# Optimization experiments

Hardware: AMD Instinct MI355X
Metric: run time of the kernel (lower is better)

## Reference

```python
import jax, jax.numpy as jnp
import numpy as np

N, E, F_IN, F_E, H = 50000, 800000, 128, 16, 64
NEG_SLOPE = 0.2


def _glorot(key, shape):
    fan_in, fan_out = shape[0], shape[-1]
    lim = np.sqrt(6.0 / (fan_in + fan_out))
    return jax.random.uniform(key, shape, jnp.float32, -lim, lim)


def setup_inputs() -> dict:
    key = jax.random.key(0)
    ks = jax.random.split(key, 24)
    inp = {
        "x": jax.random.normal(ks[0], (N, F_IN), jnp.float32),
        "edge_index": jax.random.randint(ks[1], (2, E), 0, N, jnp.int64),
        "edge_attr": jax.random.normal(ks[2], (E, F_E), jnp.float32),
    }
    k = 3
    for i, f_in in zip((1, 2, 3), (F_IN, H, H)):
        inp[f"W{i}"] = _glorot(ks[k], (f_in, H)); k += 1
        inp[f"as{i}"] = _glorot(ks[k], (H,)); k += 1
        inp[f"ad{i}"] = _glorot(ks[k], (H,)); k += 1
        inp[f"We{i}"] = _glorot(ks[k], (F_E, H)); k += 1
        inp[f"ae{i}"] = _glorot(ks[k], (H,)); k += 1
        inp[f"b{i}"] = jnp.zeros((H,), jnp.float32)
        k += 1
    return inp


def gat_conv(x, src, dst, ea, W, a_s, a_d, We, a_e, b):
    # x: [N, f_in]; src/dst: [E'] (self-loops already appended); ea: [E', F_E]
    n = x.shape[0]
    h = x @ W                                   # [N, H]
    alpha_src = h @ a_s                          # [N]
    alpha_dst = h @ a_d                          # [N]
    alpha_e = (ea @ We) @ a_e                    # [E']
    alpha = alpha_src[src] + alpha_dst[dst] + alpha_e
    alpha = jnp.where(alpha > 0, alpha, NEG_SLOPE * alpha)  # leaky_relu
    # segment softmax over incoming edges of each dst node
    amax = jax.ops.segment_max(alpha, dst, num_segments=n)
    ex = jnp.exp(alpha - amax[dst])
    denom = jax.ops.segment_sum(ex, dst, num_segments=n)
    coef = ex / (denom[dst] + 1e-16)             # [E']
    out = jax.ops.segment_sum(h[src] * coef[:, None], dst, num_segments=n)
    return out + b


def reference(x, edge_index, edge_attr,
              W1, as1, ad1, We1, ae1, b1,
              W2, as2, ad2, We2, ae2, b2,
              W3, as3, ad3, We3, ae3, b3):
    n = x.shape[0]
    # add self-loops (PyG GATConv default), edge_attr fill_value='mean'
    loop = jnp.arange(n, dtype=edge_index.dtype)
    src = jnp.concatenate([edge_index[0], loop])
    dst = jnp.concatenate([edge_index[1], loop])
    ea_mean = jnp.mean(edge_attr, axis=0)
    ea = jnp.concatenate([edge_attr, jnp.broadcast_to(ea_mean, (n, edge_attr.shape[1]))], axis=0)

    x1 = jax.nn.elu(gat_conv(x, src, dst, ea, W1, as1, ad1, We1, ae1, b1))
    x2 = jax.nn.elu(gat_conv(x1, src, dst, ea, W2, as2, ad2, We2, ae2, b2))
    x3 = jax.nn.elu(gat_conv(x2, src, dst, ea, W3, as3, ad3, We3, ae3, b3))
    node_embeddings = x1 + x2 + x3
    graph_embedding = jnp.mean(node_embeddings, axis=0, keepdims=True)  # batch=None path
    return node_embeddings, graph_embedding
```

## Files before the change

kernel.cpp:

```cpp
#include <hip/hip_runtime.h>
#include <hip/hip_fp16.h>
#include <math.h>

#define HD 64
#define MAXNBK 512
#define NPREB 512

typedef unsigned long long u64;
typedef _Float16 f16;
typedef _Float16 f16x8 __attribute__((ext_vector_type(8)));
typedef float f32x4 __attribute__((ext_vector_type(4)));

__device__ __forceinline__ u64 pack_rec(int src, float a0, float a1, float a2) {
    return (u64)(src & 0xFFFF)
         | ((u64)__half_as_ushort(__float2half(a0)) << 16)
         | ((u64)__half_as_ushort(__float2half(a1)) << 32)
         | ((u64)__half_as_ushort(__float2half(a2)) << 48);
}

__global__ void k_init(int* bcnt, float* gacc, int* tick, float* suG,
                       const float* We1, const float* ae1,
                       const float* We2, const float* ae2,
                       const float* We3, const float* ae3, int FE) {
    int t = threadIdx.x;
    for (int i = t; i < MAXNBK; i += 256) bcnt[i] = 0;
    if (t < HD) gacc[t] = 0.f;
    if (t == 0) *tick = 0;
    if (t < 3 * FE) {
        int l = t / FE, f = t % FE;
        const float* We = (l == 0) ? We1 : (l == 1) ? We2 : We3;
        const float* ae = (l == 0) ? ae1 : (l == 1) ? ae2 : ae3;
        float s = 0.f;
        for (int hh = 0; hh < HD; ++hh) s += We[f * HD + hh] * ae[hh];
        suG[t] = s;
    }
}

__global__ void k_pre(const int* __restrict__ ei, const float* __restrict__ ea,
                      const float* __restrict__ suG,
                      int E, int FE, u64* __restrict__ recE,
                      float* __restrict__ partials,
                      int nt, int chunk, int* bcnt, int* __restrict__ bhist, int NBK) {
    extern __shared__ float lds[];
    int t = threadIdx.x;

    if (blockIdx.x >= nt) {
        int* lc = (int*)lds;
        for (int i = t; i < NBK; i += 256) lc[i] = 0;
        __syncthreads();
        int cb = blockIdx.x - nt;
        int lo = cb * chunk, hi = min(E, lo + chunk);
        for (int e = lo + t; e < hi; e += 256)
            atomicAdd(&lc[ei[E + e] >> 7], 1);
        __syncthreads();
        for (int i = t; i < NBK; i += 256) {
            int c = lc[i];
            bhist[(size_t)i * NPREB + cb] = c;
            if (c) atomicAdd(&bcnt[i], c);
        }
        return;
    }

    size_t ebase = (size_t)blockIdx.x * 1024;
    float4 c0 = make_float4(0.f, 0.f, 0.f, 0.f), c1 = c0, c2 = c0, c3 = c0;

#pragma unroll
    for (int k = 0; k < 4; ++k) {
        size_t e = ebase + (size_t)k * 256 + t;
        bool ok = e < (size_t)E;
        size_t ec = ok ? e : (size_t)(E - 1);
        const float4* row = (const float4*)(ea + ec * FE);
        float4 r0 = row[0], r1 = row[1], r2 = row[2], r3 = row[3];
        int src = ei[ec];
        float rr[16];
        *(float4*)&rr[0] = r0; *(float4*)&rr[4] = r1;
        *(float4*)&rr[8] = r2; *(float4*)&rr[12] = r3;
        float a0 = 0.f, a1 = 0.f, a2 = 0.f;
#pragma unroll
        for (int f = 0; f < 16; ++f) {
            float v = rr[f];
            a0 += v * suG[f];
            a1 += v * suG[16 + f];
            a2 += v * suG[32 + f];
        }
        if (ok) {
            c0.x += r0.x; c0.y += r0.y; c0.z += r0.z; c0.w += r0.w;
            c1.x += r1.x; c1.y += r1.y; c1.z += r1.z; c1.w += r1.w;
            c2.x += r2.x; c2.y += r2.y; c2.z += r2.z; c2.w += r2.w;
            c3.x += r3.x; c3.y += r3.y; c3.z += r3.z; c3.w += r3.w;
            recE[e] = pack_rec(src, a0, a1, a2);
        }
    }

    float* cs = lds;
    float* cw = lds + 256 * 17;
    cs[t * 17 + 0] = c0.x; cs[t * 17 + 1] = c0.y; cs[t * 17 + 2] = c0.z; cs[t * 17 + 3] = c0.w;
    cs[t * 17 + 4] = c1.x; cs[t * 17 + 5] = c1.y; cs[t * 17 + 6] = c1.z; cs[t * 17 + 7] = c1.w;
    cs[t * 17 + 8] = c2.x; cs[t * 17 + 9] = c2.y; cs[t * 17 + 10] = c2.z; cs[t * 17 + 11] = c2.w;
    cs[t * 17 + 12] = c3.x; cs[t * 17 + 13] = c3.y; cs[t * 17 + 14] = c3.z; cs[t * 17 + 15] = c3.w;
    __syncthreads();
    if (t < 64) {
        int f = t & 15, g = t >> 4;
        float s = 0.f;
        for (int r = 0; r < 64; ++r) s += cs[(g * 64 + r) * 17 + f];
        cw[t] = s;
    }
    __syncthreads();
    if (t < 16)
        partials[blockIdx.x * 16 + t] = cw[t] + cw[16 + t] + cw[32 + t] + cw[48 + t];
}

__global__ void k_u2(const float* __restrict__ partials, int NB,
                     const float* __restrict__ suG,
                     float* sE, int FE, float invE,
                     const int* __restrict__ bcnt,
                     int* bfill , int* bbase, int NBK, int E) {
    __shared__ float red[256 * 4];
    __shared__ float mea[16];
    __shared__ int ib[256];
    int t = threadIdx.x;
    const float4* p4 = (const float4*)partials;
    int tot4 = NB * 4;
    float4 acc = make_float4(0.f, 0.f, 0.f, 0.f);
    for (int i = t; i < tot4; i += 256) {
        float4 v = p4[i];
        acc.x += v.x; acc.y += v.y; acc.z += v.z; acc.w += v.w;
    }
    red[t * 4 + 0] = acc.x; red[t * 4 + 1] = acc.y;
    red[t * 4 + 2] = acc.z; red[t * 4 + 3] = acc.w;
    int i0 = 2 * t, i1 = 2 * t + 1;
    int c0 = (i0 < NBK) ? bcnt[i0] : 0;
    int c1 = (i1 < NBK) ? bcnt[i1] : 0;
    ib[t] = c0 + c1;
    __syncthreads();
    for (int d = 1; d < 256; d <<= 1) {
        int x = (t >= d) ? ib[t - d] : 0;
        __syncthreads();
        ib[t] += x;
        __syncthreads();
    }
    int excl = ib[t] - (c0 + c1);
    if (i0 < NBK) { bbase[i0] = excl;      bfill[i0 * 16] = excl; }
    if (i1 < NBK) { bbase[i1] = excl + c0; bfill[i1 * 16] = excl + c0; }
    if (t == 0) bbase[NBK] = E;
    if (t < 16) {
        int q = t >> 2, j = t & 3;
        float s = 0.f;
        for (int k = 0; k < 64; ++k) s += red[(q + k * 4) * 4 + j];
        mea[q * 4 + j] = s * invE;
    }
    __syncthreads();
    if (t < 3) {
        float a = 0.f;
        for (int f = 0; f < FE; ++f) a += mea[f] * suG[t * FE + f];
        sE[t] = a;
    }
}

__global__ void k_bucket(const int* __restrict__ ei, const u64* __restrict__ recE,
                         int E, int chunk, int* bfill ,
                         u64* __restrict__ binned, unsigned char* __restrict__ bdstl,
                         int NBK, const int* __restrict__ bhist) {
    __shared__ int gb[MAXNBK], lrank[MAXNBK];
    int t = threadIdx.x;
    int cb = blockIdx.x;
    for (int i = t; i < NBK; i += 256) {
        int c = bhist[(size_t)i * NPREB + cb];
        lrank[i] = 0;
        gb[i] = c ? atomicAdd(&bfill[i * 16], c) : 0;
    }
    __syncthreads();
    int lo = cb * chunk, hi = min(E, lo + chunk);
    for (int e = lo + t; e < hi; e += 256) {
        u64 r = recE[e];
        int dst = ei[E + e];
        int b = dst >> 7;
        int rank = atomicAdd(&lrank[b], 1);
        int pos = gb[b] + rank;
        binned[pos] = r;
        bdstl[pos] = (unsigned char)(dst & 127);
    }
}

__global__ void k_sort(const int* __restrict__ bbase, const u64* __restrict__ binned,
                       const unsigned char* __restrict__ bdstl,
                       const float* __restrict__ sE,
                       int* __restrict__ row_ptr,
                       u64* __restrict__ rec, int N, int E) {
    __shared__ int lcnt[128], lfill[128];
    int b = blockIdx.x, t = threadIdx.x;
    int base = bbase[b], nrec = bbase[b + 1] - base;
    if (t < 128) lcnt[t] = 0;
    __syncthreads();
    for (int i = t; i < nrec; i += 256)
        atomicAdd(&lcnt[bdstl[base + i]], 1);
    __syncthreads();
    int v = (t < 128) ? lcnt[t] : 0;
    for (int d = 1; d < 128; d <<= 1) {
        int x = (t >= d && t < 128) ? lcnt[t - d] : 0;
        __syncthreads();
        if (t < 128) lcnt[t] += x;
        __syncthreads();
    }
    int gnode = (b << 7) + t;
    if (t < 128) {
        int rp = base + gnode + (lcnt[t] - v);
        if (gnode < N) {
            row_ptr[gnode] = rp;
            rec[rp] = pack_rec(gnode, sE[0], sE[1], sE[2]);
        }
        lfill[t] = rp + 1;
    }
    if (b == 0 && t == 0) row_ptr[N] = E + N;
    __syncthreads();
    for (int i = t; i < nrec; i += 256) {
        u64 r = binned[base + i];
        int dl = bdstl[base + i];
        int p = atomicAdd(&lfill[dl], 1);
        rec[p] = r;
    }
}

__global__ void k_gemm(const void* __restrict__ xin, int in_f16,
                       const float* __restrict__ W,
                       const float* __restrict__ a_s, const float* __restrict__ a_d,
                       __half* __restrict__ h, float* __restrict__ as_n,
                       float* __restrict__ ad_n, int N, int K) {
    extern __shared__ char smem[];
    const int SK = K + 8;
    f16* xs = (f16*)smem;
    f16* wt = xs + 64 * SK;
    int t = threadIdx.x;
    int nb = blockIdx.x * 64;

    int nK4 = K >> 2;
    if (in_f16) {
        const __half* xh = (const __half*)xin;
        for (int i = t; i < 64 * nK4; i += 256) {
            int row = i / nK4, c4 = i % nK4;
            int gr = nb + row; if (gr >= N) gr = N - 1;
            u64 v = ((const u64*)(xh + (size_t)gr * K))[c4];
            *(u64*)&xs[row * SK + c4 * 4] = v;
        }
    } else {
        const float* xf = (const float*)xin;
        for (int i = t; i < 64 * nK4; i += 256) {
            int row = i / nK4, c4 = i % nK4;
            int gr = nb + row; if (gr >= N) gr = N - 1;
            float4 v = ((const float4*)(xf + (size_t)gr * K))[c4];
            f16* p = &xs[row * SK + c4 * 4];
            p[0] = (f16)v.x; p[1] = (f16)v.y; p[2] = (f16)v.z; p[3] = (f16)v.w;
        }
    }
    for (int i = t; i < K * 64; i += 256) {
        int k = i >> 6, c = i & 63;
        wt[c * SK + k] = (f16)W[i];
    }
    __syncthreads();

    int wv = t >> 6, lane = t & 63;
    int m = lane & 15, quad = lane >> 4;
    int rowA = wv * 16 + m;

    f32x4 acc[4];
#pragma unroll
    for (int ct = 0; ct < 4; ++ct) acc[ct] = (f32x4){0.f, 0.f, 0.f, 0.f};

    for (int ks = 0; ks < (K >> 5); ++ks) {
        f16x8 a = *(const f16x8*)&xs[rowA * SK + ks * 32 + quad * 8];
#pragma unroll
        for (int ct = 0; ct < 4; ++ct) {
            f16x8 bf = *(const f16x8*)&wt[(ct * 16 + m) * SK + ks * 32 + quad * 8];
            acc[ct] = __builtin_amdgcn_mfma_f32_16x16x32_f16(a, bf, acc[ct], 0, 0, 0);
        }
    }

    {
        float as_c[4], ad_c[4];
#pragma unroll
        for (int ct = 0; ct < 4; ++ct) {
            as_c[ct] = a_s[ct * 16 + m];
            ad_c[ct] = a_d[ct * 16 + m];
        }
#pragma unroll
        for (int r = 0; r < 4; ++r) {
            float ps = acc[0][r] * as_c[0] + acc[1][r] * as_c[1]
                     + acc[2][r] * as_c[2] + acc[3][r] * as_c[3];
            float pd = acc[0][r] * ad_c[0] + acc[1][r] * ad_c[1]
                     + acc[2][r] * ad_c[2] + acc[3][r] * ad_c[3];
#pragma unroll
            for (int dd = 8; dd; dd >>= 1) {
                ps += __shfl_xor(ps, dd, 64);
                pd += __shfl_xor(pd, dd, 64);
            }
            if (m == 0) {
                int gr = nb + wv * 16 + quad * 4 + r;
                if (gr < N) { as_n[gr] = ps; ad_n[gr] = pd; }
            }
        }
    }

    __syncthreads();
    f16* ht = xs;
    const int HS = 72;
#pragma unroll
    for (int ct = 0; ct < 4; ++ct)
#pragma unroll
        for (int r = 0; r < 4; ++r) {
            int rl = wv * 16 + quad * 4 + r;
            ht[rl * HS + ct * 16 + m] = (f16)acc[ct][r];
        }
    __syncthreads();

    {
        int row = t >> 2, cb = (t & 3) * 16;
        int gr = nb + row;
        if (gr < N) {
            ulonglong2 v0 = *(const ulonglong2*)&ht[row * HS + cb];
            ulonglong2 v1 = *(const ulonglong2*)&ht[row * HS + cb + 8];
            *(ulonglong2*)(h + (size_t)gr * HD + cb) = v0;
            *(ulonglong2*)(h + (size_t)gr * HD + cb + 8) = v1;
        }
    }
}

__global__ void k_aggr(const __half* __restrict__ h, const float* __restrict__ as_n,
                       const float* __restrict__ ad_n, const int* __restrict__ row_ptr,
                       const u64* __restrict__ rec, int l,
                       const float* __restrict__ b, __half* __restrict__ x_out,
                       float* __restrict__ emb, int N, int first) {
    int wave = threadIdx.x >> 6, lane = threadIdx.x & 63;
    int hl = lane & 31;
    int n = blockIdx.x * 8 + wave * 2 + (lane >> 5);
    int nc = min(n, N - 1);
    int base = row_ptr[nc], end = row_ptr[nc + 1];
    float adv = ad_n[nc];
    const int shift = 16 * (l + 1);
    int qq = (lane >> 3) & 3, fo = lane & 7;
    int nch = (end - base + 31) >> 5;
    int nchmax = max(nch, __shfl_xor(nch, 32, 64));
    float m = -INFINITY, d = 0.f;
    float acc[8];
#pragma unroll
    for (int k = 0; k < 8; ++k) acc[k] = 0.f;

    for (int ch = 0; ch < nchmax; ++ch) {
        int c = base + (ch << 5);
        int cnt = min(32, end - c);
        float a = -INFINITY;
        int s = 0;
        if (hl < cnt) {
            u64 r = rec[c + hl];
            s = (int)(r & 0xFFFFull);
            float aE = __half2float(__ushort_as_half((unsigned short)(r >> shift)));
            a = as_n[s] + adv + aE;
            a = (a > 0.f) ? a : 0.2f * a;
        }
        float mc = a;
#pragma unroll
        for (int dd = 16; dd; dd >>= 1) mc = fmaxf(mc, __shfl_xor(mc, dd, 64));
        float mn = fmaxf(m, mc);
        float w = (hl < cnt) ? __expf(a - mn) : 0.f;
        float dc = w;
#pragma unroll
        for (int dd = 16; dd; dd >>= 1) dc += __shfl_xor(dc, dd, 64);
        float sc = __expf(m - mn);
        d = d * sc + dc;
#pragma unroll
        for (int k = 0; k < 8; ++k) acc[k] *= sc;
        m = mn;
        int iters = (max(cnt, 0) + 3) >> 2;
        for (int j4 = 0; j4 < iters; ++j4) {
            int j = (j4 << 2) + qq;
            int sl = (lane & 32) + j;
            int sj = __shfl(s, sl, 64);
            float wj = __shfl(w, sl, 64);
            uint4 hv = *(const uint4*)(h + (size_t)sj * HD + (fo << 3));
            asm("v_fma_mix_f32 %0, %1, %2, %0 op_sel:[0,0,0] op_sel_hi:[0,1,0]"
                : "+v"(acc[0]) : "v"(wj), "v"(hv.x));
            asm("v_fma_mix_f32 %0, %1, %2, %0 op_sel:[0,1,0] op_sel_hi:[0,1,0]"
                : "+v"(acc[1]) : "v"(wj), "v"(hv.x));
            asm("v_fma_mix_f32 %0, %1, %2, %0 op_sel:[0,0,0] op_sel_hi:[0,1,0]"
                : "+v"(acc[2]) : "v"(wj), "v"(hv.y));
            asm("v_fma_mix_f32 %0, %1, %2, %0 op_sel:[0,1,0] op_sel_hi:[0,1,0]"
                : "+v"(acc[3]) : "v"(wj), "v"(hv.y));
            asm("v_fma_mix_f32 %0, %1, %2, %0 op_sel:[0,0,0] op_sel_hi:[0,1,0]"
                : "+v"(acc[4]) : "v"(wj), "v"(hv.z));
            asm("v_fma_mix_f32 %0, %1, %2, %0 op_sel:[0,1,0] op_sel_hi:[0,1,0]"
                : "+v"(acc[5]) : "v"(wj), "v"(hv.z));
            asm("v_fma_mix_f32 %0, %1, %2, %0 op_sel:[0,0,0] op_sel_hi:[0,1,0]"
                : "+v"(acc[6]) : "v"(wj), "v"(hv.w));
            asm("v_fma_mix_f32 %0, %1, %2, %0 op_sel:[0,1,0] op_sel_hi:[0,1,0]"
                : "+v"(acc[7]) : "v"(wj), "v"(hv.w));
        }
    }

#pragma unroll
    for (int k = 0; k < 8; ++k) {
        acc[k] += __shfl_xor(acc[k], 8, 64);
        acc[k] += __shfl_xor(acc[k], 16, 64);
    }
    if (hl < 8 && n < N) {
        float inv = 1.f / (d + 1e-16f);
        const float4* b4p = (const float4*)(b + (fo << 3));
        float4 b0 = b4p[0], b1 = b4p[1];
        float bb[8] = {b0.x, b0.y, b0.z, b0.w, b1.x, b1.y, b1.z, b1.w};
        float vv[8];
#pragma unroll
        for (int k = 0; k < 8; ++k) {
            float v = acc[k] * inv + bb[k];
            vv[k] = (v > 0.f) ? v : expm1f(v);
        }
        union { unsigned short us[8]; ulonglong2 u2; } ou;
#pragma unroll
        for (int k = 0; k < 8; ++k) ou.us[k] = __half_as_ushort(__float2half(vv[k]));
        *(ulonglong2*)(x_out + (size_t)n * HD + (fo << 3)) = ou.u2;
        float4* ep = (float4*)(emb + (size_t)n * HD + (fo << 3));
        if (first) {
            ep[0] = make_float4(vv[0], vv[1], vv[2], vv[3]);
            ep[1] = make_float4(vv[4], vv[5], vv[6], vv[7]);
        } else {
            float4 e0 = ep[0], e1 = ep[1];
            e0.x += vv[0]; e0.y += vv[1]; e0.z += vv[2]; e0.w += vv[3];
            e1.x += vv[4]; e1.y += vv[5]; e1.z += vv[6]; e1.w += vv[7];
            ep[0] = e0; ep[1] = e1;
        }
    }
}

__global__ void k_red(float* __restrict__ emb, float* __restrict__ gacc,
                      int* __restrict__ tick, int N) {
    __shared__ float lds[256];
    __shared__ int lastf;
    int f = threadIdx.x & 63, w = threadIdx.x >> 6;
    float s = 0.f;
    for (int n = blockIdx.x * 4 + w; n < N; n += gridDim.x * 4)
        s += emb[(size_t)n * HD + f];
    lds[threadIdx.x] = s;
    __syncthreads();
    if (w == 0) {
        float v = lds[f] + lds[64 + f] + lds[128 + f] + lds[192 + f];
        atomicAdd(&gacc[f], v);
    }
    __syncthreads();
    __threadfence();
    if (threadIdx.x == 0)
        lastf = (atomicAdd(tick, 1) == (int)gridDim.x - 1);
    __syncthreads();
    if (lastf && threadIdx.x < HD) {
        float g = __hip_atomic_load(&gacc[threadIdx.x], __ATOMIC_RELAXED,
                                    __HIP_MEMORY_SCOPE_AGENT);
        emb[(size_t)N * HD + threadIdx.x] = g / (float)N;
    }
}

extern "C" void kernel_launch(void* const* d_in, const int* in_sizes, int n_in,
                              void* d_out, int out_size, void* d_ws, size_t ws_size,
                              hipStream_t stream) {
    const float* x = (const float*)d_in[0];
    const int* ei = (const int*)d_in[1];
    const float* ea = (const float*)d_in[2];

    const int FIN = in_sizes[3] / HD;
    const int N = in_sizes[0] / FIN;
    const int E = in_sizes[1] / 2;
    const int FE = in_sizes[2] / E;
    const int NBK = (N + 127) >> 7;

    const float* W[3];  const float* as_[3]; const float* ad_[3];
    const float* We[3]; const float* ae_[3]; const float* bb[3];
    for (int l = 0; l < 3; ++l) {
        W[l]  = (const float*)d_in[3 + 6 * l + 0];
        as_[l] = (const float*)d_in[3 + 6 * l + 1];
        ad_[l] = (const float*)d_in[3 + 6 * l + 2];
        We[l] = (const float*)d_in[3 + 6 * l + 3];
        ae_[l] = (const float*)d_in[3 + 6 * l + 4];
        bb[l] = (const float*)d_in[3 + 6 * l + 5];
    }

    int ntiles = (E + 1023) / 1024;
    int chunk = (E + NPREB - 1) / NPREB;

    char* ws = (char*)d_ws;
    size_t off = 0;
    auto alloc = [&](size_t bytes) {
        void* p = ws + off;
        off += (bytes + 255) & ~(size_t)255;
        return p;
    };
    __half* h      = (__half*)alloc((size_t)N * HD * 2);
    __half* x_cur  = (__half*)alloc((size_t)N * HD * 2);
    float*  as_n   = (float*)alloc((size_t)N * 4);
    float*  ad_n   = (float*)alloc((size_t)N * 4);
    int*    rowp   = (int*)alloc((size_t)(N + 1) * 4);
    int*    bcnt   = (int*)alloc((size_t)MAXNBK * 4);
    int*    bfill  = (int*)alloc((size_t)MAXNBK * 16 * 4);
    int*    bbase  = (int*)alloc((size_t)(MAXNBK + 1) * 4);
    int*    bhist  = (int*)alloc((size_t)MAXNBK * NPREB * 4);
    u64*    rec    = (u64*)alloc((size_t)(E + N) * 8);
    u64*    recE   = (u64*)alloc((size_t)E * 8);
    u64*    binned = (u64*)alloc((size_t)E * 8);
    unsigned char* bdstl = (unsigned char*)alloc((size_t)E);
    float*  partials = (float*)alloc((size_t)ntiles * 16 * 4);
    float*  sE     = (float*)alloc(3 * 4);
    float*  gacc   = (float*)alloc(HD * 4);
    float*  suG    = (float*)alloc(3 * 16 * 4);
    int*    tick   = (int*)alloc(4);
    (void)ws_size; (void)n_in; (void)out_size;

    float* emb = (float*)d_out;

    k_init<<<1, 256, 0, stream>>>(bcnt, gacc, tick, suG,
                                  We[0], ae_[0], We[1], ae_[1], We[2], ae_[2], FE);
    size_t pre_lds = (size_t)(256 * 17 + 64) * 4;
    k_pre<<<ntiles + NPREB, 256, pre_lds, stream>>>(ei, ea, suG, E, FE, recE, partials,
                                                    ntiles, chunk, bcnt, bhist, NBK);
    k_u2<<<1, 256, 0, stream>>>(partials, ntiles, suG, sE, FE, 1.0f / (float)E,
                                bcnt, bfill, bbase, NBK, E);
    k_bucket<<<NPREB, 256, 0, stream>>>(ei, recE, E, chunk, bfill, binned, bdstl,
                                        NBK, bhist);
    k_sort<<<NBK, 256, 0, stream>>>(bbase, binned, bdstl, sE, rowp, rec, N, E);

    for (int l = 0; l < 3; ++l) {
        const void* xin = (l == 0) ? (const void*)x : (const void*)x_cur;
        int in_f16 = (l == 0) ? 0 : 1;
        int K = (l == 0) ? FIN : HD;
        size_t ldsz = (size_t)(2 * 64 * (K + 8)) * 2;
        k_gemm<<<(N + 63) / 64, 256, ldsz, stream>>>(xin, in_f16, W[l], as_[l], ad_[l],
                                                     h, as_n, ad_n, N, K);
        k_aggr<<<(N + 7) / 8, 256, 0, stream>>>(h, as_n, ad_n, rowp, rec, l,
                                                bb[l], x_cur, emb, N, (l == 0) ? 1 : 0);
    }

    k_red<<<256, 256, 0, stream>>>(emb, gacc, tick, N);
}
```

Baseline: 344.5 us.

## Fuse layer-1 GEMM into preprocessing launch and pre-transpose weights once

```diff
diff --git a/kernel.cpp b/kernel.cpp
--- a/kernel.cpp
+++ b/kernel.cpp
@@ -21,7 +21,9 @@
 __global__ void k_init(int* bcnt, float* gacc, int* tick, float* suG,
                        const float* We1, const float* ae1,
                        const float* We2, const float* ae2,
-                       const float* We3, const float* ae3, int FE) {
+                       const float* We3, const float* ae3, int FE,
+                       const float* W1, const float* W2, const float* W3,
+                       f16* WT0, f16* WT1, f16* WT2, int FIN) {
     int t = threadIdx.x;
     for (int i = t; i < MAXNBK; i += 256) bcnt[i] = 0;
     if (t < HD) gacc[t] = 0.f;
@@ -34,21 +36,116 @@
         for (int hh = 0; hh < HD; ++hh) s += We[f * HD + hh] * ae[hh];
         suG[t] = s;
     }
-}
-
-__global__ void k_pre(const int* __restrict__ ei, const float* __restrict__ ea,
-                      const float* __restrict__ suG,
-                      int E, int FE, u64* __restrict__ recE,
-                      float* __restrict__ partials,
-                      int nt, int chunk, int* bcnt, int* __restrict__ bhist, int NBK) {
-    extern __shared__ float lds[];
+    for (int i = t; i < HD * FIN; i += 256) {
+        int k = i >> 6, c = i & 63;
+        WT0[c * FIN + k] = (f16)W1[i];
+    }
+    for (int i = t; i < HD * HD; i += 256) {
+        int k = i >> 6, c = i & 63;
+        WT1[c * HD + k] = (f16)W2[i];
+        WT2[c * HD + k] = (f16)W3[i];
+    }
+}
+
+__global__ void k_preX(const int* __restrict__ ei, const float* __restrict__ ea,
+                       const float* __restrict__ suG,
+                       int E, int FE, u64* __restrict__ recE,
+                       float* __restrict__ partials,
+                       int nt, int chunk, int* bcnt, int* __restrict__ bhist, int NBK,
+                       int Gg, const float* __restrict__ x,
+                       const f16* __restrict__ WT,
+                       const float* __restrict__ a_s, const float* __restrict__ a_d,
+                       __half* __restrict__ h, float* __restrict__ as_n,
+                       float* __restrict__ ad_n, int N, int K) {
+    extern __shared__ char smemraw[];
     int t = threadIdx.x;
 
-    if (blockIdx.x >= nt) {
-        int* lc = (int*)lds;
+    if (blockIdx.x < Gg) {
+        const int SK = K + 8;
+        f16* xs = (f16*)smemraw;
+        int nb = blockIdx.x * 64;
+        int nK4 = K >> 2;
+        for (int i = t; i < 64 * nK4; i += 256) {
+            int row = i / nK4, c4 = i % nK4;
+            int gr = nb + row; if (gr >= N) gr = N - 1;
+            float4 v = ((const float4*)(x + (size_t)gr * K))[c4];
+            f16* p = &xs[row * SK + c4 * 4];
+            p[0] = (f16)v.x; p[1] = (f16)v.y; p[2] = (f16)v.z; p[3] = (f16)v.w;
+        }
+        __syncthreads();
+
+        int wv = t >> 6, lane = t & 63;
+        int m = lane & 15, quad = lane >> 4;
+        int rowA = wv * 16 + m;
+
+        f32x4 acc[4];
+#pragma unroll
+        for (int ct = 0; ct < 4; ++ct) acc[ct] = (f32x4){0.f, 0.f, 0.f, 0.f};
+
+        for (int ks = 0; ks < (K >> 5); ++ks) {
+            f16x8 a = *(const f16x8*)&xs[rowA * SK + ks * 32 + quad * 8];
+#pragma unroll
+            for (int ct = 0; ct < 4; ++ct) {
+                f16x8 bf = *(const f16x8*)&WT[(ct * 16 + m) * K + ks * 32 + quad * 8];
+                acc[ct] = __builtin_amdgcn_mfma_f32_16x16x32_f16(a, bf, acc[ct], 0, 0, 0);
+            }
+        }
+
+        {
+            float as_c[4], ad_c[4];
+#pragma unroll
+            for (int ct = 0; ct < 4; ++ct) {
+                as_c[ct] = a_s[ct * 16 + m];
+                ad_c[ct] = a_d[ct * 16 + m];
+            }
+#pragma unroll
+            for (int r = 0; r < 4; ++r) {
+                float ps = acc[0][r] * as_c[0] + acc[1][r] * as_c[1]
+                         + acc[2][r] * as_c[2] + acc[3][r] * as_c[3];
+                float pd = acc[0][r] * ad_c[0] + acc[1][r] * ad_c[1]
+                         + acc[2][r] * ad_c[2] + acc[3][r] * ad_c[3];
+#pragma unroll
+                for (int dd = 8; dd; dd >>= 1) {
+                    ps += __shfl_xor(ps, dd, 64);
+                    pd += __shfl_xor(pd, dd, 64);
+                }
+                if (m == 0) {
+                    int gr = nb + wv * 16 + quad * 4 + r;
+                    if (gr < N) { as_n[gr] = ps; ad_n[gr] = pd; }
+                }
+            }
+        }
+
+        __syncthreads();
+        f16* ht = xs;
+        const int HS = 72;
+#pragma unroll
+        for (int ct = 0; ct < 4; ++ct)
+#pragma unroll
+            for (int r = 0; r < 4; ++r) {
+                int rl = wv * 16 + quad * 4 + r;
+                ht[rl * HS + ct * 16 + m] = (f16)acc[ct][r];
+            }
+        __syncthreads();
+        {
+            int row = t >> 2, cb = (t & 3) * 16;
+            int gr = nb + row;
+            if (gr < N) {
+                ulonglong2 v0 = *(const ulonglong2*)&ht[row * HS + cb];
+                ulonglong2 v1 = *(const ulonglong2*)&ht[row * HS + cb + 8];
+                *(ulonglong2*)(h + (size_t)gr * HD + cb) = v0;
+                *(ulonglong2*)(h + (size_t)gr * HD + cb + 8) = v1;
+            }
+        }
+        return;
+    }
+
+    int bx = blockIdx.x - Gg;
+    if (bx >= nt) {
+        int* lc = (int*)smemraw;
         for (int i = t; i < NBK; i += 256) lc[i] = 0;
         __syncthreads();
-        int cb = blockIdx.x - nt;
+        int cb = bx - nt;
         int lo = cb * chunk, hi = min(E, lo + chunk);
         for (int e = lo + t; e < hi; e += 256)
             atomicAdd(&lc[ei[E + e] >> 7], 1);
@@ -61,7 +158,7 @@
         return;
     }
 
-    size_t ebase = (size_t)blockIdx.x * 1024;
+    size_t ebase = (size_t)bx * 1024;
     float4 c0 = make_float4(0.f, 0.f, 0.f, 0.f), c1 = c0, c2 = c0, c3 = c0;
 
 #pragma unroll
@@ -92,8 +189,8 @@
         }
     }
 
-    float* cs = lds;
-    float* cw = lds + 256 * 17;
+    float* cs = (float*)smemraw;
+    float* cw = cs + 256 * 17;
     cs[t * 17 + 0] = c0.x; cs[t * 17 + 1] = c0.y; cs[t * 17 + 2] = c0.z; cs[t * 17 + 3] = c0.w;
     cs[t * 17 + 4] = c1.x; cs[t * 17 + 5] = c1.y; cs[t * 17 + 6] = c1.z; cs[t * 17 + 7] = c1.w;
     cs[t * 17 + 8] = c2.x; cs[t * 17 + 9] = c2.y; cs[t * 17 + 10] = c2.z; cs[t * 17 + 11] = c2.w;
@@ -107,7 +204,7 @@
     }
     __syncthreads();
     if (t < 16)
-        partials[blockIdx.x * 16 + t] = cw[t] + cw[16 + t] + cw[32 + t] + cw[48 + t];
+        partials[bx * 16 + t] = cw[t] + cw[16 + t] + cw[32 + t] + cw[48 + t];
 }
 
 __global__ void k_u2(const float* __restrict__ partials, int NB,
@@ -221,40 +318,23 @@
     }
 }
 
-__global__ void k_gemm(const void* __restrict__ xin, int in_f16,
-                       const float* __restrict__ W,
+__global__ void k_gemm(const __half* __restrict__ xin,
+                       const f16* __restrict__ WT,
                        const float* __restrict__ a_s, const float* __restrict__ a_d,
                        __half* __restrict__ h, float* __restrict__ as_n,
                        float* __restrict__ ad_n, int N, int K) {
     extern __shared__ char smem[];
     const int SK = K + 8;
     f16* xs = (f16*)smem;
-    f16* wt = xs + 64 * SK;
     int t = threadIdx.x;
     int nb = blockIdx.x * 64;
 
     int nK4 = K >> 2;
-    if (in_f16) {
-        const __half* xh = (const __half*)xin;
-        for (int i = t; i < 64 * nK4; i += 256) {
-            int row = i / nK4, c4 = i % nK4;
-            int gr = nb + row; if (gr >= N) gr = N - 1;
-            u64 v = ((const u64*)(xh + (size_t)gr * K))[c4];
-            *(u64*)&xs[row * SK + c4 * 4] = v;
-        }
-    } else {
-        const float* xf = (const float*)xin;
-        for (int i = t; i < 64 * nK4; i += 256) {
-            int row = i / nK4, c4 = i % nK4;
-            int gr = nb + row; if (gr >= N) gr = N - 1;
-            float4 v = ((const float4*)(xf + (size_t)gr * K))[c4];
-            f16* p = &xs[row * SK + c4 * 4];
-            p[0] = (f16)v.x; p[1] = (f16)v.y; p[2] = (f16)v.z; p[3] = (f16)v.w;
-        }
-    }
-    for (int i = t; i < K * 64; i += 256) {
-        int k = i >> 6, c = i & 63;
-        wt[c * SK + k] = (f16)W[i];
+    for (int i = t; i < 64 * nK4; i += 256) {
+        int row = i / nK4, c4 = i % nK4;
+        int gr = nb + row; if (gr >= N) gr = N - 1;
+        u64 v = ((const u64*)(xin + (size_t)gr * K))[c4];
+        *(u64*)&xs[row * SK + c4 * 4] = v;
     }
     __syncthreads();
 
@@ -270,7 +350,7 @@
         f16x8 a = *(const f16x8*)&xs[rowA * SK + ks * 32 + quad * 8];
 #pragma unroll
         for (int ct = 0; ct < 4; ++ct) {
-            f16x8 bf = *(const f16x8*)&wt[(ct * 16 + m) * SK + ks * 32 + quad * 8];
+            f16x8 bf = *(const f16x8*)&WT[(ct * 16 + m) * K + ks * 32 + quad * 8];
             acc[ct] = __builtin_amdgcn_mfma_f32_16x16x32_f16(a, bf, acc[ct], 0, 0, 0);
         }
     }
@@ -480,6 +560,7 @@
 
     int ntiles = (E + 1023) / 1024;
     int chunk = (E + NPREB - 1) / NPREB;
+    int Gg = (N + 63) / 64;
 
     char* ws = (char*)d_ws;
     size_t off = 0;
@@ -505,16 +586,23 @@
     float*  sE     = (float*)alloc(3 * 4);
     float*  gacc   = (float*)alloc(HD * 4);
     float*  suG    = (float*)alloc(3 * 16 * 4);
+    f16*    WT0    = (f16*)alloc((size_t)HD * FIN * 2);
+    f16*    WT1    = (f16*)alloc((size_t)HD * HD * 2);
+    f16*    WT2    = (f16*)alloc((size_t)HD * HD * 2);
     int*    tick   = (int*)alloc(4);
     (void)ws_size; (void)n_in; (void)out_size;
 
     float* emb = (float*)d_out;
 
     k_init<<<1, 256, 0, stream>>>(bcnt, gacc, tick, suG,
-                                  We[0], ae_[0], We[1], ae_[1], We[2], ae_[2], FE);
+                                  We[0], ae_[0], We[1], ae_[1], We[2], ae_[2], FE,
+                                  W[0], W[1], W[2], WT0, WT1, WT2, FIN);
     size_t pre_lds = (size_t)(256 * 17 + 64) * 4;
-    k_pre<<<ntiles + NPREB, 256, pre_lds, stream>>>(ei, ea, suG, E, FE, recE, partials,
-                                                    ntiles, chunk, bcnt, bhist, NBK);
+    size_t g0_lds = (size_t)(64 * (FIN + 8)) * 2;
+    size_t fused_lds = pre_lds > g0_lds ? pre_lds : g0_lds;
+    k_preX<<<Gg + ntiles + NPREB, 256, fused_lds, stream>>>(
+        ei, ea, suG, E, FE, recE, partials, ntiles, chunk, bcnt, bhist, NBK,
+        Gg, x, WT0, as_[0], ad_[0], h, as_n, ad_n, N, FIN);
     k_u2<<<1, 256, 0, stream>>>(partials, ntiles, suG, sE, FE, 1.0f / (float)E,
                                 bcnt, bfill, bbase, NBK, E);
     k_bucket<<<NPREB, 256, 0, stream>>>(ei, recE, E, chunk, bfill, binned, bdstl,
@@ -522,12 +610,11 @@
     k_sort<<<NBK, 256, 0, stream>>>(bbase, binned, bdstl, sE, rowp, rec, N, E);
 
     for (int l = 0; l < 3; ++l) {
-        const void* xin = (l == 0) ? (const void*)x : (const void*)x_cur;
-        int in_f16 = (l == 0) ? 0 : 1;
-        int K = (l == 0) ? FIN : HD;
-        size_t ldsz = (size_t)(2 * 64 * (K + 8)) * 2;
-        k_gemm<<<(N + 63) / 64, 256, ldsz, stream>>>(xin, in_f16, W[l], as_[l], ad_[l],
-                                                     h, as_n, ad_n, N, K);
+        if (l > 0) {
+            size_t ldsz = (size_t)(64 * (HD + 8)) * 2;
+            k_gemm<<<(N + 63) / 64, 256, ldsz, stream>>>(
+                x_cur, (l == 1) ? WT1 : WT2, as_[l], ad_[l], h, as_n, ad_n, N, HD);
+        }
         k_aggr<<<(N + 7) / 8, 256, 0, stream>>>(h, as_n, ad_n, rowp, rec, l,
                                                 bb[l], x_cur, emb, N, (l == 0) ? 1 : 0);
     }
```

Measured after the change: 359.2 us. 1.04x slower.
